# Kernel optimization log

Hardware: AMD Instinct MI355X
Metric: run time of the kernel (lower is better)

Reference implementation:

```python
import jax, jax.numpy as jnp
import numpy as np

EPS = 1e-6
B, I, N, Wd, R = 128, 512, 512, 32, 4


def setup_inputs() -> dict:
    key = jax.random.key(0)
    ks = jax.random.split(key, 32)
    inp = {
        "xi": jax.random.normal(ks[0], (B, I), jnp.float32),
        "memory": jax.random.normal(ks[1], (B, N, Wd), jnp.float32),
        "link_matrix": jax.random.uniform(ks[2], (B, N, N), jnp.float32),
        "precedence": jax.random.uniform(ks[3], (B, N), jnp.float32),
        "read_weights": jax.random.uniform(ks[4], (B, R, N), jnp.float32),
        "write_weights": jax.random.uniform(ks[5], (B, N), jnp.float32),
        "usage": jax.random.uniform(ks[6], (B, N), jnp.float32),
    }
    # 10 independent linear heads (weight [out, in], bias [out]) as in independent_linears=True
    dims = [("rk", R * Wd), ("rs", R), ("wk", Wd), ("ws", 1), ("ev", Wd),
            ("wv", Wd), ("fg", R), ("ag", 1), ("wg", 1), ("rm", 3 * R)]
    scale = 1.0 / np.sqrt(I).astype(np.float32)
    for i, (nm, d) in enumerate(dims):
        inp["W_" + nm] = jax.random.normal(ks[7 + 2 * i], (d, I), jnp.float32) * scale
        inp["b_" + nm] = jax.random.normal(ks[8 + 2 * i], (d,), jnp.float32) * 0.01
    return inp


def reference(xi, memory, link_matrix, precedence, read_weights, write_weights, usage,
              W_rk, b_rk, W_rs, b_rs, W_wk, b_wk, W_ws, b_ws, W_ev, b_ev,
              W_wv, b_wv, W_fg, b_fg, W_ag, b_ag, W_wg, b_wg, W_rm, b_rm):
    b, n, w = memory.shape
    r = b_rs.shape[0]
    lin = lambda Wm, bm: xi @ Wm.T + bm

    # interface vectors
    read_keys = jnp.tanh(lin(W_rk, b_rk)).reshape(b, r, w)          # [B,R,W]
    read_str = jax.nn.softplus(lin(W_rs, b_rs))                      # [B,R]
    write_key = jnp.tanh(lin(W_wk, b_wk))                            # [B,W]
    write_str = jax.nn.softplus(lin(W_ws, b_ws))                     # [B,1]
    erase = jax.nn.sigmoid(lin(W_ev, b_ev))                          # [B,W]
    write_vec = jnp.tanh(lin(W_wv, b_wv))                            # [B,W]
    free = jax.nn.sigmoid(lin(W_fg, b_fg))                           # [B,R]
    alloc_g = jax.nn.sigmoid(lin(W_ag, b_ag))                        # [B,1]
    write_g = jax.nn.sigmoid(lin(W_wg, b_wg))                        # [B,1]
    modes = jax.nn.softmax(lin(W_rm, b_rm).reshape(b, r, 3), axis=2)

    # usage update (memory retention)
    psi = jnp.prod(1.0 - free[:, :, None] * read_weights, axis=1)    # [B,N]
    usage = (usage + write_weights - usage * write_weights) * psi

    # allocation weighting via sorted usage
    idx = jnp.argsort(usage, axis=1)
    su = jnp.take_along_axis(usage, idx, axis=1)
    prod_excl = jnp.concatenate(
        [jnp.ones((b, 1), su.dtype), jnp.cumprod(su, axis=1)[:, :-1]], axis=1)
    alloc_sorted = (1.0 - su) * prod_excl
    alloc = jnp.zeros_like(usage).at[jnp.arange(b)[:, None], idx].set(alloc_sorted)

    # write content addressing (cosine similarity)
    mem_norm = jnp.linalg.norm(memory, axis=2)                       # [B,N]
    wsim = jnp.einsum('bnw,bw->bn', memory, write_key) / (
        mem_norm * jnp.linalg.norm(write_key, axis=1, keepdims=True) + EPS)
    wc = jax.nn.softmax(write_str * wsim, axis=1)                    # [B,N]

    ww = write_g * (alloc_g * alloc + (1.0 - alloc_g) * wc)          # [B,N]

    # memory write (erase then add)
    memory = memory * (1.0 - ww[:, :, None] * erase[:, None, :]) \
             + ww[:, :, None] * write_vec[:, None, :]

    # temporal link matrix + precedence update
    link = (1.0 - ww[:, :, None] - ww[:, None, :]) * link_matrix \
           + ww[:, :, None] * precedence[:, None, :]
    link = link * (1.0 - jnp.eye(n, dtype=link.dtype))
    precedence = (1.0 - jnp.sum(ww, axis=1, keepdims=True)) * precedence + ww

    # directional read weights from previous read weights
    fw = jnp.einsum('bnm,brm->brn', link, read_weights)              # forward: L w
    bw = jnp.einsum('bmn,brm->brn', link, read_weights)              # backward: L^T w

    # read content addressing on updated memory
    mem_norm2 = jnp.linalg.norm(memory, axis=2)
    rsim = jnp.einsum('bnw,brw->brn', memory, read_keys) / (
        mem_norm2[:, None, :] * jnp.linalg.norm(read_keys, axis=2, keepdims=True) + EPS)
    rc = jax.nn.softmax(read_str[:, :, None] * rsim, axis=2)         # [B,R,N]

    read_weights = modes[:, :, 0:1] * bw + modes[:, :, 1:2] * rc + modes[:, :, 2:3] * fw
    read_vectors = jnp.einsum('brn,bnw->brw', read_weights, memory)  # [B,R,W]
    return read_vectors, memory, link, precedence, read_weights, ww, usage
```

## Files before the change

### kernel.cpp

```cpp
#include <hip/hip_runtime.h>
#include <math.h>

#define BB 128
#define ID 512
#define NN 512
#define WDIM 32
#define RR 4
#define EPSF 1e-6f
#define NTILE 16

#define OFF_RV   ((size_t)0)
#define OFF_MEM  (OFF_RV + (size_t)BB*RR*WDIM)
#define OFF_LINK (OFF_MEM + (size_t)BB*NN*WDIM)
#define OFF_PREC (OFF_LINK + (size_t)BB*NN*NN)
#define OFF_RW   (OFF_PREC + (size_t)BB*NN)
#define OFF_WW   (OFF_RW + (size_t)BB*RR*NN)
#define OFF_USG  (OFF_WW + (size_t)BB*NN)

#define IF_RK 0
#define IF_RS 128
#define IF_WK 132
#define IF_WS 164
#define IF_EV 165
#define IF_WV 197
#define IF_FG 229
#define IF_AG 233
#define IF_WG 234
#define IF_RM 235

#define WS_IFACE ((size_t)0)
#define WS_FW    (WS_IFACE + (size_t)BB*256)
#define WS_BW    (WS_FW + (size_t)BB*RR*NN)
#define WS_PART  WS_BW
#define WS_PART_FLOATS ((size_t)BB*NTILE*RR*NN)

__device__ __forceinline__ float sigm(float x) { return 1.0f / (1.0f + expf(-x)); }
__device__ __forceinline__ float softplusf(float x) { return fmaxf(x, 0.0f) + log1pf(expf(-fabsf(x))); }

struct HeadArgs {
  const float *Wrk, *brk, *Wrs, *brs, *Wwk, *bwk, *Wws, *bws, *Wev, *bev,
              *Wwv, *bwv, *Wfg, *bfg, *Wag, *bag, *Wwg, *bwg, *Wrm, *brm;
};

__global__ __launch_bounds__(256) void k1_heads(const float* __restrict__ xi, HeadArgs ha,
                                                float* __restrict__ iface) {
  __shared__ __align__(16) float xs[ID];
  __shared__ float raw[256];
  int b = blockIdx.x, t = threadIdx.x;
  for (int i = t; i < ID; i += 256) xs[i] = xi[b * ID + i];
  __syncthreads();
  const float* Ws[10] = {ha.Wrk, ha.Wrs, ha.Wwk, ha.Wws, ha.Wev, ha.Wwv, ha.Wfg, ha.Wag, ha.Wwg, ha.Wrm};
  const float* bs[10] = {ha.brk, ha.brs, ha.bwk, ha.bws, ha.bev, ha.bwv, ha.bfg, ha.bag, ha.bwg, ha.brm};
  const int off[11] = {0, 128, 132, 164, 165, 197, 229, 233, 234, 235, 247};
  float val = 0.0f;
  int h = -1, row = 0;
  if (t < 247) {
    for (int k = 0; k < 10; ++k)
      if (t >= off[k] && t < off[k + 1]) { h = k; row = t - off[k]; }
    const float4* w4 = (const float4*)(Ws[h] + row * ID);
    const float4* x4 = (const float4*)xs;
    float acc = 0.0f;
    for (int i = 0; i < ID / 4; ++i) {
      float4 w = w4[i], x = x4[i];
      acc += w.x * x.x + w.y * x.y + w.z * x.z + w.w * x.w;
    }
    val = acc + bs[h][row];
  }
  raw[t] = val;
  __syncthreads();
  if (t < 247) {
    float o;
    if (h == 0 || h == 2 || h == 5) o = tanhf(val);
    else if (h == 1 || h == 3) o = softplusf(val);
    else if (h == 9) {
      int g = (t - 235) / 3;
      float a0 = raw[235 + g * 3], a1 = raw[236 + g * 3], a2 = raw[237 + g * 3];
      float mx = fmaxf(a0, fmaxf(a1, a2));
      o = expf(val - mx) / (expf(a0 - mx) + expf(a1 - mx) + expf(a2 - mx));
    } else o = sigm(val);
    iface[b * 256 + t] = o;
  }
}

__global__ __launch_bounds__(512) void k2_write(const float* __restrict__ mem_in,
                                                const float* __restrict__ prec_in,
                                                const float* __restrict__ rw_in,
                                                const float* __restrict__ wwt_in,
                                                const float* __restrict__ usg_in,
                                                const float* __restrict__ iface,
                                                float* __restrict__ bw,
                                                float* __restrict__ out) {
  __shared__ __align__(16) float sif[256];
  __shared__ float sv[NN];
  __shared__ int si[NN];
  __shared__ float salloc[NN];
  __shared__ float sred[8];
  __shared__ float swt[8];
  int b = blockIdx.x, tid = threadIdx.x;
  int lane = tid & 63, wave = tid >> 6;

  for (int i = tid; i < RR * NN; i += 512) bw[(size_t)b * RR * NN + i] = 0.0f;

  if (tid < 256) sif[tid] = iface[b * 256 + tid];
  __syncthreads();

  const float* rwb = rw_in + (size_t)b * RR * NN;
  float psi = 1.0f;
#pragma unroll
  for (int r = 0; r < RR; r++) psi *= 1.0f - sif[IF_FG + r] * rwb[r * NN + tid];
  float u = usg_in[b * NN + tid], wwt = wwt_in[b * NN + tid];
  u = (u + wwt - u * wwt) * psi;

  float v = u; int idx = tid;
  for (int k = 2; k <= NN; k <<= 1) {
    for (int j = k >> 1; j > 0; j >>= 1) {
      int p = tid ^ j;
      float pv; int pi;
      if (j >= 64) {
        sv[tid] = v; si[tid] = idx;
        __syncthreads();
        pv = sv[p]; pi = si[p];
        __syncthreads();
      } else {
        pv = __shfl_xor(v, j);
        pi = __shfl_xor(idx, j);
      }
      bool mineSmaller = (v < pv) || (v == pv && idx < pi);
      bool keepMin = (((tid & k) == 0) == (tid < p));
      bool take = keepMin ? !mineSmaller : mineSmaller;
      if (take) { v = pv; idx = pi; }
    }
  }

  float pr = v;
#pragma unroll
  for (int o = 1; o < 64; o <<= 1) {
    float q = __shfl_up(pr, o);
    if (lane >= o) pr *= q;
  }
  if (lane == 63) swt[wave] = pr;
  __syncthreads();
  float wp = 1.0f;
#pragma unroll
  for (int w = 0; w < 8; w++) if (w < wave) wp *= swt[w];
  float ep = __shfl_up(pr, 1);
  if (lane == 0) ep = 1.0f;
  float alloc_sorted = (1.0f - v) * (wp * ep);
  salloc[idx] = alloc_sorted;
  __syncthreads();
  float alloc = salloc[tid];

  const float4* mrow = (const float4*)(mem_in + ((size_t)b * NN + tid) * WDIM);
  float4 mv[8];
  float dot = 0, nrm = 0, wkn = 0;
#pragma unroll
  for (int i = 0; i < 8; i++) {
    float4 m = mrow[i];
    mv[i] = m;
    const float4 kk = *(const float4*)&sif[IF_WK + 4 * i];
    dot += m.x * kk.x + m.y * kk.y + m.z * kk.z + m.w * kk.w;
    nrm += m.x * m.x + m.y * m.y + m.z * m.z + m.w * m.w;
    wkn += kk.x * kk.x + kk.y * kk.y + kk.z * kk.z + kk.w * kk.w;
  }
  float s = sif[IF_WS] * (dot / (sqrtf(nrm) * sqrtf(wkn) + EPSF));

  float m8 = s;
#pragma unroll
  for (int d = 32; d > 0; d >>= 1) m8 = fmaxf(m8, __shfl_down(m8, d));
  if (lane == 0) sred[wave] = m8;
  __syncthreads();
  float mx = sred[0];
#pragma unroll
  for (int w = 1; w < 8; w++) mx = fmaxf(mx, sred[w]);
  __syncthreads();
  float e = expf(s - mx);
  float sm = e;
#pragma unroll
  for (int d = 32; d > 0; d >>= 1) sm += __shfl_down(sm, d);
  if (lane == 0) sred[wave] = sm;
  __syncthreads();
  float esum = 0;
#pragma unroll
  for (int w = 0; w < 8; w++) esum += sred[w];
  __syncthreads();
  float wc = e / esum;

  float ww = sif[IF_WG] * (sif[IF_AG] * alloc + (1.0f - sif[IF_AG]) * wc);
  out[OFF_WW + b * NN + tid] = ww;
  out[OFF_USG + b * NN + tid] = u;

  float ws_ = ww;
#pragma unroll
  for (int d = 32; d > 0; d >>= 1) ws_ += __shfl_down(ws_, d);
  if (lane == 0) sred[wave] = ws_;
  __syncthreads();
  float wsum = 0;
#pragma unroll
  for (int w = 0; w < 8; w++) wsum += sred[w];
  out[OFF_PREC + b * NN + tid] = (1.0f - wsum) * prec_in[b * NN + tid] + ww;

  float* mo = out + OFF_MEM + ((size_t)b * NN + tid) * WDIM;
#pragma unroll
  for (int i = 0; i < 8; i++) {
    float4 m = mv[i];
    float4 o;
    o.x = m.x * (1.0f - ww * sif[IF_EV + 4 * i + 0]) + ww * sif[IF_WV + 4 * i + 0];
    o.y = m.y * (1.0f - ww * sif[IF_EV + 4 * i + 1]) + ww * sif[IF_WV + 4 * i + 1];
    o.z = m.z * (1.0f - ww * sif[IF_EV + 4 * i + 2]) + ww * sif[IF_WV + 4 * i + 2];
    o.w = m.w * (1.0f - ww * sif[IF_EV + 4 * i + 3]) + ww * sif[IF_WV + 4 * i + 3];
    ((float4*)mo)[i] = o;
  }
}

template<int PARTIAL>
__global__ __launch_bounds__(256) void k3_link(const float* __restrict__ link_in,
                                               const float* __restrict__ prec_in,
                                               const float* __restrict__ rw_in,
                                               const float* __restrict__ ww_out,
                                               float* __restrict__ link_out,
                                               float* __restrict__ fw,
                                               float* __restrict__ bw) {
  __shared__ __align__(16) float sww[NN];
  __shared__ __align__(16) float sprec[NN];
  __shared__ __align__(16) float srw[RR * NN];
  __shared__ float sbw[RR * NN];
  __shared__ float sfw[RR * 32];
  int b = blockIdx.y, tile = blockIdx.x, tid = threadIdx.x;
  for (int i = tid; i < NN; i += 256) {
    sww[i] = ww_out[b * NN + i];
    sprec[i] = prec_in[b * NN + i];
  }
  for (int i = tid; i < RR * NN; i += 256) {
    srw[i] = rw_in[(size_t)b * RR * NN + i];
    sbw[i] = 0.0f;
  }
  __syncthreads();

  int wave = tid >> 6, lane = tid & 63;
  float4 cww[2], cpr[2], crw[RR][2];
#pragma unroll
  for (int h = 0; h < 2; h++) {
    cww[h] = ((const float4*)sww)[h * 64 + lane];
    cpr[h] = ((const float4*)sprec)[h * 64 + lane];
#pragma unroll
    for (int r = 0; r < RR; r++) crw[r][h] = ((const float4*)(srw + r * NN))[h * 64 + lane];
  }

  float bwa[RR][8];
#pragma unroll
  for (int r = 0; r < RR; r++)
#pragma unroll
    for (int j = 0; j < 8; j++) bwa[r][j] = 0.0f;

  const size_t lbase = (size_t)b * NN * NN;
  const float* lbp = link_in + lbase;
  int row0 = tile * 32 + wave;

  float4 nv0 = ((const float4*)(lbp + (size_t)row0 * NN))[lane];
  float4 nv1 = ((const float4*)(lbp + (size_t)row0 * NN))[64 + lane];

  for (int i = 0; i < 8; i++) {
    int row = row0 + 4 * i;
    float4 cv[2] = {nv0, nv1};
    if (i < 7) {
      const float4* Ln = (const float4*)(lbp + (size_t)(row + 4) * NN);
      nv0 = Ln[lane];
      nv1 = Ln[64 + lane];
    }
    float wwr = sww[row];
    float rwr[RR] = {srw[row], srw[NN + row], srw[2 * NN + row], srw[3 * NN + row]};
    float4* Lo = (float4*)(link_out + lbase + (size_t)row * NN);
    float fp[RR] = {0, 0, 0, 0};
#pragma unroll
    for (int h = 0; h < 2; h++) {
      float4 lv = cv[h];
      float l[4] = {lv.x, lv.y, lv.z, lv.w};
      float wc[4] = {cww[h].x, cww[h].y, cww[h].z, cww[h].w};
      float pc[4] = {cpr[h].x, cpr[h].y, cpr[h].z, cpr[h].w};
      int c0 = h * 256 + 4 * lane;
#pragma unroll
      for (int j = 0; j < 4; j++) {
        float ln = (1.0f - wwr - wc[j]) * l[j] + wwr * pc[j];
        if (c0 + j == row) ln = 0.0f;
        l[j] = ln;
#pragma unroll
        for (int r = 0; r < RR; r++) bwa[r][h * 4 + j] += ln * rwr[r];
      }
#pragma unroll
      for (int r = 0; r < RR; r++) {
        float rc0 = (r == 0) ? crw[0][h].x : (r == 1) ? crw[1][h].x : (r == 2) ? crw[2][h].x : crw[3][h].x;
        float rc1 = (r == 0) ? crw[0][h].y : (r == 1) ? crw[1][h].y : (r == 2) ? crw[2][h].y : crw[3][h].y;
        float rc2 = (r == 0) ? crw[0][h].z : (r == 1) ? crw[1][h].z : (r == 2) ? crw[2][h].z : crw[3][h].z;
        float rc3 = (r == 0) ? crw[0][h].w : (r == 1) ? crw[1][h].w : (r == 2) ? crw[2][h].w : crw[3][h].w;
        fp[r] += l[0] * rc0 + l[1] * rc1 + l[2] * rc2 + l[3] * rc3;
      }
      float4 ov = {l[0], l[1], l[2], l[3]};
      Lo[h * 64 + lane] = ov;
    }
#pragma unroll
    for (int d = 32; d > 0; d >>= 1) {
      fp[0] += __shfl_down(fp[0], d);
      fp[1] += __shfl_down(fp[1], d);
      fp[2] += __shfl_down(fp[2], d);
      fp[3] += __shfl_down(fp[3], d);
    }
    if (lane == 0) {
      int rl = wave + 4 * i;
      sfw[0 * 32 + rl] = fp[0];
      sfw[1 * 32 + rl] = fp[1];
      sfw[2 * 32 + rl] = fp[2];
      sfw[3 * 32 + rl] = fp[3];
    }
  }
  __syncthreads();

  if (tid < RR * 32) {
    int r = tid >> 5, j = tid & 31;
    fw[(size_t)b * RR * NN + r * NN + tile * 32 + j] = sfw[tid];
  }

  for (int w = 0; w < 4; w++) {
    if (wave == w) {
#pragma unroll
      for (int r = 0; r < RR; r++)
#pragma unroll
        for (int h = 0; h < 2; h++)
#pragma unroll
          for (int j = 0; j < 4; j++)
            sbw[r * NN + h * 256 + 4 * lane + j] += bwa[r][h * 4 + j];
    }
    __syncthreads();
  }
  if (PARTIAL) {
    float* bp = bw + ((size_t)(b * NTILE + tile)) * RR * NN;
    for (int i = tid; i < RR * NN; i += 256) bp[i] = sbw[i];
  } else {
    float* bp = bw + (size_t)b * RR * NN;
    for (int i = tid; i < RR * NN; i += 256) atomicAdd(&bp[i], sbw[i]);
  }
}

template<int PARTIAL>
__global__ __launch_bounds__(512) void k4_read(const float* __restrict__ iface,
                                               const float* __restrict__ fw,
                                               const float* __restrict__ bw,
                                               float* __restrict__ out) {
  __shared__ __align__(16) float srk[WDIM];
  __shared__ float sred[8];
  __shared__ float srwn[NN];
  __shared__ float spart[16][WDIM];
  int b = blockIdx.x >> 2, r = blockIdx.x & 3;
  int tid = threadIdx.x, lane = tid & 63, wave = tid >> 6;
  const float* ifb = iface + b * 256;
  if (tid < WDIM) srk[tid] = ifb[IF_RK + r * WDIM + tid];
  __syncthreads();
  float rkn2 = 0;
#pragma unroll
  for (int w = 0; w < WDIM; w++) { float v = srk[w]; rkn2 += v * v; }
  float rkn = sqrtf(rkn2);

  const float* mem = out + OFF_MEM + (size_t)b * NN * WDIM;
  const float4* mrow = (const float4*)(mem + (size_t)tid * WDIM);
  float d = 0, nrm = 0;
#pragma unroll
  for (int i = 0; i < 8; i++) {
    float4 m = mrow[i];
    const float4 kk = *(const float4*)&srk[4 * i];
    nrm += m.x * m.x + m.y * m.y + m.z * m.z + m.w * m.w;
    d += m.x * kk.x + m.y * kk.y + m.z * kk.z + m.w * kk.w;
  }
  float s = ifb[IF_RS + r] * (d / (sqrtf(nrm) * rkn + EPSF));

  float m8 = s;
#pragma unroll
  for (int dd = 32; dd > 0; dd >>= 1) m8 = fmaxf(m8, __shfl_down(m8, dd));
  if (lane == 0) sred[wave] = m8;
  __syncthreads();
  float mx = sred[0];
#pragma unroll
  for (int w = 1; w < 8; w++) mx = fmaxf(mx, sred[w]);
  __syncthreads();
  float e = expf(s - mx);
  float sm = e;
#pragma unroll
  for (int dd = 32; dd > 0; dd >>= 1) sm += __shfl_down(sm, dd);
  if (lane == 0) sred[wave] = sm;
  __syncthreads();
  float esum = 0;
#pragma unroll
  for (int w = 0; w < 8; w++) esum += sred[w];
  float rc = e / esum;

  float bwv;
  if (PARTIAL) {
    const float* pp = bw + ((size_t)b * NTILE * RR + r) * NN + tid;
    float acc = 0.0f;
#pragma unroll
    for (int t = 0; t < NTILE; t++) acc += pp[(size_t)t * RR * NN];
    bwv = acc;
  } else {
    bwv = bw[((size_t)b * RR + r) * NN + tid];
  }
  float fwv = fw[((size_t)b * RR + r) * NN + tid];
  float m0 = ifb[IF_RM + 3 * r], m1 = ifb[IF_RM + 3 * r + 1], m2 = ifb[IF_RM + 3 * r + 2];
  float v = m0 * bwv + m1 * rc + m2 * fwv;
  srwn[tid] = v;
  out[OFF_RW + ((size_t)b * RR + r) * NN + tid] = v;
  __syncthreads();

  int w = tid & 31, part = tid >> 5;
  float acc = 0;
  const float* mp = mem + (size_t)part * 32 * WDIM + w;
  const float* rp = srwn + part * 32;
#pragma unroll
  for (int n = 0; n < 32; n++) acc += rp[n] * mp[(size_t)n * WDIM];
  spart[part][w] = acc;
  __syncthreads();
  if (tid < WDIM) {
    float vv = 0;
#pragma unroll
    for (int p = 0; p < 16; p++) vv += spart[p][tid];
    out[OFF_RV + ((size_t)b * RR + r) * WDIM + tid] = vv;
  }
}

extern "C" void kernel_launch(void* const* d_in, const int* in_sizes, int n_in,
                              void* d_out, int out_size, void* d_ws, size_t ws_size,
                              hipStream_t stream) {
  const float* xi = (const float*)d_in[0];
  const float* mem = (const float*)d_in[1];
  const float* link = (const float*)d_in[2];
  const float* prec = (const float*)d_in[3];
  const float* rw = (const float*)d_in[4];
  const float* wwt = (const float*)d_in[5];
  const float* usg = (const float*)d_in[6];
  HeadArgs ha;
  ha.Wrk = (const float*)d_in[7];  ha.brk = (const float*)d_in[8];
  ha.Wrs = (const float*)d_in[9];  ha.brs = (const float*)d_in[10];
  ha.Wwk = (const float*)d_in[11]; ha.bwk = (const float*)d_in[12];
  ha.Wws = (const float*)d_in[13]; ha.bws = (const float*)d_in[14];
  ha.Wev = (const float*)d_in[15]; ha.bev = (const float*)d_in[16];
  ha.Wwv = (const float*)d_in[17]; ha.bwv = (const float*)d_in[18];
  ha.Wfg = (const float*)d_in[19]; ha.bfg = (const float*)d_in[20];
  ha.Wag = (const float*)d_in[21]; ha.bag = (const float*)d_in[22];
  ha.Wwg = (const float*)d_in[23]; ha.bwg = (const float*)d_in[24];
  ha.Wrm = (const float*)d_in[25]; ha.brm = (const float*)d_in[26];

  float* out = (float*)d_out;
  float* ws = (float*)d_ws;
  float* iface = ws + WS_IFACE;
  float* fwbuf = ws + WS_FW;
  float* bwbuf = ws + WS_BW;

  const size_t need_part_bytes = (WS_PART + WS_PART_FLOATS) * sizeof(float);
  const bool use_partial = ws_size >= need_part_bytes;

  k1_heads<<<BB, 256, 0, stream>>>(xi, ha, iface);
  k2_write<<<BB, 512, 0, stream>>>(mem, prec, rw, wwt, usg, iface, bwbuf, out);
  if (use_partial) {
    k3_link<1><<<dim3(NTILE, BB), 256, 0, stream>>>(link, prec, rw, out + OFF_WW, out + OFF_LINK, fwbuf, ws + WS_PART);
    k4_read<1><<<BB * RR, 512, 0, stream>>>(iface, fwbuf, ws + WS_PART, out);
  } else {
    k3_link<0><<<dim3(NTILE, BB), 256, 0, stream>>>(link, prec, rw, out + OFF_WW, out + OFF_LINK, fwbuf, bwbuf);
    k4_read<0><<<BB * RR, 512, 0, stream>>>(iface, fwbuf, bwbuf, out);
  }
}
```

Before: 352.6 us.

## Restructure link kernel: 512 threads, upfront row loads, nontemporal stores, LDS atomics

The link-update kernel now runs 512 threads per block. Each pair of waves owns 8 rows, and each wave of the pair covers one half of the columns. All 8 rows' link values are loaded into registers before the shared-memory setup, so global load latency overlaps the staging. Output stores use nontemporal hints to avoid polluting the cache. The serialized per-wave bw accumulation loop is replaced with LDS atomics, and forward partial sums are combined with LDS atomics, trading sync barriers for atomic contention and more registers per thread.

```diff
diff --git a/kernel.cpp b/kernel.cpp
--- a/kernel.cpp
+++ b/kernel.cpp
@@ -8,6 +8,8 @@
 #define RR 4
 #define EPSF 1e-6f
 #define NTILE 16
+
+typedef float nt_float4 __attribute__((ext_vector_type(4)));
 
 #define OFF_RV   ((size_t)0)
 #define OFF_MEM  (OFF_RV + (size_t)BB*RR*WDIM)
@@ -213,90 +215,83 @@
 }
 
 template<int PARTIAL>
-__global__ __launch_bounds__(256) void k3_link(const float* __restrict__ link_in,
-                                               const float* __restrict__ prec_in,
-                                               const float* __restrict__ rw_in,
-                                               const float* __restrict__ ww_out,
-                                               float* __restrict__ link_out,
-                                               float* __restrict__ fw,
-                                               float* __restrict__ bw) {
+__global__ __launch_bounds__(512, 4) void k3_link(const float* __restrict__ link_in,
+                                                  const float* __restrict__ prec_in,
+                                                  const float* __restrict__ rw_in,
+                                                  const float* __restrict__ ww_out,
+                                                  float* __restrict__ link_out,
+                                                  float* __restrict__ fw,
+                                                  float* __restrict__ bw) {
   __shared__ __align__(16) float sww[NN];
   __shared__ __align__(16) float sprec[NN];
   __shared__ __align__(16) float srw[RR * NN];
   __shared__ float sbw[RR * NN];
   __shared__ float sfw[RR * 32];
   int b = blockIdx.y, tile = blockIdx.x, tid = threadIdx.x;
-  for (int i = tid; i < NN; i += 256) {
+  int wave = tid >> 6, lane = tid & 63;
+  int g = wave >> 1;
+  int ch = wave & 1;
+  int row0 = tile * 32 + g * 8;
+  const size_t lbase = (size_t)b * NN * NN;
+  const float* lbp = link_in + lbase;
+
+  float4 pl[8];
+#pragma unroll
+  for (int i = 0; i < 8; i++)
+    pl[i] = ((const float4*)(lbp + (size_t)(row0 + i) * NN))[ch * 64 + lane];
+
+  for (int i = tid; i < NN; i += 512) {
     sww[i] = ww_out[b * NN + i];
     sprec[i] = prec_in[b * NN + i];
   }
-  for (int i = tid; i < RR * NN; i += 256) {
+  for (int i = tid; i < RR * NN; i += 512) {
     srw[i] = rw_in[(size_t)b * RR * NN + i];
     sbw[i] = 0.0f;
   }
-  __syncthreads();
-
-  int wave = tid >> 6, lane = tid & 63;
-  float4 cww[2], cpr[2], crw[RR][2];
-#pragma unroll
-  for (int h = 0; h < 2; h++) {
-    cww[h] = ((const float4*)sww)[h * 64 + lane];
-    cpr[h] = ((const float4*)sprec)[h * 64 + lane];
-#pragma unroll
-    for (int r = 0; r < RR; r++) crw[r][h] = ((const float4*)(srw + r * NN))[h * 64 + lane];
-  }
-
-  float bwa[RR][8];
+  if (tid < RR * 32) sfw[tid] = 0.0f;
+  __syncthreads();
+
+  int c0 = ch * 256 + 4 * lane;
+  float4 cww = ((const float4*)sww)[ch * 64 + lane];
+  float4 cpr = ((const float4*)sprec)[ch * 64 + lane];
+  float4 crw[RR];
+#pragma unroll
+  for (int r = 0; r < RR; r++) crw[r] = ((const float4*)(srw + r * NN))[ch * 64 + lane];
+
+  float bwa[RR][4];
 #pragma unroll
   for (int r = 0; r < RR; r++)
 #pragma unroll
-    for (int j = 0; j < 8; j++) bwa[r][j] = 0.0f;
-
-  const size_t lbase = (size_t)b * NN * NN;
-  const float* lbp = link_in + lbase;
-  int row0 = tile * 32 + wave;
-
-  float4 nv0 = ((const float4*)(lbp + (size_t)row0 * NN))[lane];
-  float4 nv1 = ((const float4*)(lbp + (size_t)row0 * NN))[64 + lane];
-
+    for (int j = 0; j < 4; j++) bwa[r][j] = 0.0f;
+
+  float wcc[4] = {cww.x, cww.y, cww.z, cww.w};
+  float pcc[4] = {cpr.x, cpr.y, cpr.z, cpr.w};
+
+#pragma unroll
   for (int i = 0; i < 8; i++) {
-    int row = row0 + 4 * i;
-    float4 cv[2] = {nv0, nv1};
-    if (i < 7) {
-      const float4* Ln = (const float4*)(lbp + (size_t)(row + 4) * NN);
-      nv0 = Ln[lane];
-      nv1 = Ln[64 + lane];
-    }
+    int row = row0 + i;
     float wwr = sww[row];
     float rwr[RR] = {srw[row], srw[NN + row], srw[2 * NN + row], srw[3 * NN + row]};
-    float4* Lo = (float4*)(link_out + lbase + (size_t)row * NN);
+    float l[4] = {pl[i].x, pl[i].y, pl[i].z, pl[i].w};
     float fp[RR] = {0, 0, 0, 0};
 #pragma unroll
-    for (int h = 0; h < 2; h++) {
-      float4 lv = cv[h];
-      float l[4] = {lv.x, lv.y, lv.z, lv.w};
-      float wc[4] = {cww[h].x, cww[h].y, cww[h].z, cww[h].w};
-      float pc[4] = {cpr[h].x, cpr[h].y, cpr[h].z, cpr[h].w};
-      int c0 = h * 256 + 4 * lane;
-#pragma unroll
-      for (int j = 0; j < 4; j++) {
-        float ln = (1.0f - wwr - wc[j]) * l[j] + wwr * pc[j];
-        if (c0 + j == row) ln = 0.0f;
-        l[j] = ln;
-#pragma unroll
-        for (int r = 0; r < RR; r++) bwa[r][h * 4 + j] += ln * rwr[r];
-      }
-#pragma unroll
-      for (int r = 0; r < RR; r++) {
-        float rc0 = (r == 0) ? crw[0][h].x : (r == 1) ? crw[1][h].x : (r == 2) ? crw[2][h].x : crw[3][h].x;
-        float rc1 = (r == 0) ? crw[0][h].y : (r == 1) ? crw[1][h].y : (r == 2) ? crw[2][h].y : crw[3][h].y;
-        float rc2 = (r == 0) ? crw[0][h].z : (r == 1) ? crw[1][h].z : (r == 2) ? crw[2][h].z : crw[3][h].z;
-        float rc3 = (r == 0) ? crw[0][h].w : (r == 1) ? crw[1][h].w : (r == 2) ? crw[2][h].w : crw[3][h].w;
-        fp[r] += l[0] * rc0 + l[1] * rc1 + l[2] * rc2 + l[3] * rc3;
-      }
-      float4 ov = {l[0], l[1], l[2], l[3]};
-      Lo[h * 64 + lane] = ov;
-    }
+    for (int j = 0; j < 4; j++) {
+      float ln = (1.0f - wwr - wcc[j]) * l[j] + wwr * pcc[j];
+      if (c0 + j == row) ln = 0.0f;
+      l[j] = ln;
+#pragma unroll
+      for (int r = 0; r < RR; r++) bwa[r][j] += ln * rwr[r];
+    }
+#pragma unroll
+    for (int r = 0; r < RR; r++) {
+      float rc0 = (r == 0) ? crw[0].x : (r == 1) ? crw[1].x : (r == 2) ? crw[2].x : crw[3].x;
+      float rc1 = (r == 0) ? crw[0].y : (r == 1) ? crw[1].y : (r == 2) ? crw[2].y : crw[3].y;
+      float rc2 = (r == 0) ? crw[0].z : (r == 1) ? crw[1].z : (r == 2) ? crw[2].z : crw[3].z;
+      float rc3 = (r == 0) ? crw[0].w : (r == 1) ? crw[1].w : (r == 2) ? crw[2].w : crw[3].w;
+      fp[r] = l[0] * rc0 + l[1] * rc1 + l[2] * rc2 + l[3] * rc3;
+    }
+    nt_float4 ov = {l[0], l[1], l[2], l[3]};
+    __builtin_nontemporal_store(ov, (nt_float4*)(link_out + lbase + (size_t)row * NN) + ch * 64 + lane);
 #pragma unroll
     for (int d = 32; d > 0; d >>= 1) {
       fp[0] += __shfl_down(fp[0], d);
@@ -305,13 +300,18 @@
       fp[3] += __shfl_down(fp[3], d);
     }
     if (lane == 0) {
-      int rl = wave + 4 * i;
-      sfw[0 * 32 + rl] = fp[0];
-      sfw[1 * 32 + rl] = fp[1];
-      sfw[2 * 32 + rl] = fp[2];
-      sfw[3 * 32 + rl] = fp[3];
-    }
-  }
+      int rl = g * 8 + i;
+      atomicAdd(&sfw[0 * 32 + rl], fp[0]);
+      atomicAdd(&sfw[1 * 32 + rl], fp[1]);
+      atomicAdd(&sfw[2 * 32 + rl], fp[2]);
+      atomicAdd(&sfw[3 * 32 + rl], fp[3]);
+    }
+  }
+
+#pragma unroll
+  for (int r = 0; r < RR; r++)
+#pragma unroll
+    for (int j = 0; j < 4; j++) atomicAdd(&sbw[r * NN + c0 + j], bwa[r][j]);
   __syncthreads();
 
   if (tid < RR * 32) {
@@ -319,24 +319,12 @@
     fw[(size_t)b * RR * NN + r * NN + tile * 32 + j] = sfw[tid];
   }
 
-  for (int w = 0; w < 4; w++) {
-    if (wave == w) {
-#pragma unroll
-      for (int r = 0; r < RR; r++)
-#pragma unroll
-        for (int h = 0; h < 2; h++)
-#pragma unroll
-          for (int j = 0; j < 4; j++)
-            sbw[r * NN + h * 256 + 4 * lane + j] += bwa[r][h * 4 + j];
-    }
-    __syncthreads();
-  }
   if (PARTIAL) {
     float* bp = bw + ((size_t)(b * NTILE + tile)) * RR * NN;
-    for (int i = tid; i < RR * NN; i += 256) bp[i] = sbw[i];
+    for (int i = tid; i < RR * NN; i += 512) bp[i] = sbw[i];
   } else {
     float* bp = bw + (size_t)b * RR * NN;
-    for (int i = tid; i < RR * NN; i += 256) atomicAdd(&bp[i], sbw[i]);
+    for (int i = tid; i < RR * NN; i += 512) atomicAdd(&bp[i], sbw[i]);
   }
 }
 
@@ -458,10 +446,10 @@
   k1_heads<<<BB, 256, 0, stream>>>(xi, ha, iface);
   k2_write<<<BB, 512, 0, stream>>>(mem, prec, rw, wwt, usg, iface, bwbuf, out);
   if (use_partial) {
-    k3_link<1><<<dim3(NTILE, BB), 256, 0, stream>>>(link, prec, rw, out + OFF_WW, out + OFF_LINK, fwbuf, ws + WS_PART);
+    k3_link<1><<<dim3(NTILE, BB), 512, 0, stream>>>(link, prec, rw, out + OFF_WW, out + OFF_LINK, fwbuf, ws + WS_PART);
     k4_read<1><<<BB * RR, 512, 0, stream>>>(iface, fwbuf, ws + WS_PART, out);
   } else {
-    k3_link<0><<<dim3(NTILE, BB), 256, 0, stream>>>(link, prec, rw, out + OFF_WW, out + OFF_LINK, fwbuf, bwbuf);
+    k3_link<0><<<dim3(NTILE, BB), 512, 0, stream>>>(link, prec, rw, out + OFF_WW, out + OFF_LINK, fwbuf, bwbuf);
     k4_read<0><<<BB * RR, 512, 0, stream>>>(iface, fwbuf, bwbuf, out);
   }
 }
```

Result: slower. 419.7 us (+19.0%).
